# Performance work log

Measured on AMD Instinct MI355X. Metric: run time of the kernel, lower is better.

Reference implementation:

```python
import jax, jax.numpy as jnp
import numpy as np

# Config matching init_kwargs (single TP rank: local heads == total heads)
HID = 1024
NH = 16      # query heads
NKV = 4      # kv heads (GQA)
HD = 64      # head_dim
B = 2
S = 2048
SCALE = 1.0 / HD ** 0.5


def setup_inputs() -> dict:
    key = jax.random.key(0)
    k1, k2, k3 = jax.random.split(key, 3)
    qkv_out = (NH + 2 * NKV) * HD  # 1536
    return {
        "hidden_states": jax.random.normal(k1, (B, S, HID), dtype=jnp.float32),
        "W_qkv": jax.random.normal(k2, (HID, qkv_out), dtype=jnp.float32) * 0.02,
        "W_o": jax.random.normal(k3, (HID, HID), dtype=jnp.float32) * 0.02,
    }


def reference(hidden_states, W_qkv, W_o):
    b, s, _ = hidden_states.shape
    rep = NH // NKV  # GQA repeat factor (repeat_interleave: q head h uses kv group h // rep)

    qkv = hidden_states @ W_qkv  # [B, S, (NH+2*NKV)*HD]
    q, k, v = jnp.split(qkv, [NH * HD, (NH + NKV) * HD], axis=-1)

    # [B, heads, S, HD]
    q = q.reshape(b, s, NH, HD).transpose(0, 2, 1, 3)
    k = k.reshape(b, s, NKV, HD).transpose(0, 2, 1, 3)
    v = v.reshape(b, s, NKV, HD).transpose(0, 2, 1, 3)

    # Group query heads by shared kv head instead of repeat_interleaving K/V in memory.
    qg = q.reshape(b, NKV, rep, s, HD)  # head h = g*rep + r  <=>  kv group g = h // rep
    scores = jnp.einsum("bgrqd,bgkd->bgrqk", qg, k) * SCALE  # [B, NKV, rep, S, S]

    # Causal mask (prefill path: kv_cache is None, seq_len > 1)
    causal = jnp.triu(jnp.ones((s, s), dtype=bool), k=1)
    scores = jnp.where(causal, jnp.finfo(scores.dtype).min, scores)

    attn = jax.nn.softmax(scores, axis=-1)
    out = jnp.einsum("bgrqk,bgkd->bgrqd", attn, v)  # [B, NKV, rep, S, HD]
    out = out.reshape(b, NH, s, HD).transpose(0, 2, 1, 3).reshape(b, s, NH * HD)
    return out @ W_o  # [B, S, HID]
```

## Files before the change

### kernel.cpp

```cpp
#include <hip/hip_runtime.h>
#include <stdint.h>

using u16 = unsigned short;
using u32 = unsigned int;

typedef __attribute__((ext_vector_type(8))) short short8;
typedef __attribute__((ext_vector_type(4))) float f32x4;
typedef __attribute__((ext_vector_type(16))) float f32x16;

__device__ __forceinline__ u16 f2bf(float f) {
  u32 u = __builtin_bit_cast(u32, f);
  u = (u + 0x7fffu + ((u >> 16) & 1u)) >> 16;
  return (u16)u;
}

__device__ __forceinline__ u32 cvtpk(float lo, float hi) {
  u32 r;
  asm("v_cvt_pk_bf16_f32 %0, %1, %2" : "=v"(r) : "v"(lo), "v"(hi));
  return r;
}

__device__ __forceinline__ short8 ld16(const u16* p) {
  uint4 v = *(const uint4*)p;
  union { uint4 u; short8 s; } c; c.u = v; return c.s;
}

__device__ __forceinline__ void gload_lds16(const void* g, void* l) {
  __builtin_amdgcn_global_load_lds(
      (const __attribute__((address_space(1))) void*)g,
      (__attribute__((address_space(3))) void*)l, 16, 0, 0);
}

__device__ __forceinline__ f32x16 mfma32(short8 a, short8 b, f32x16 c) {
  return __builtin_amdgcn_mfma_f32_32x32x16_bf16(a, b, c, 0, 0, 0);
}

__global__ __launch_bounds__(256) void k_prep(const float* __restrict__ hs,
                                              const float* __restrict__ wqkv,
                                              const float* __restrict__ wo,
                                              u16* __restrict__ hsb,
                                              u16* __restrict__ wqkvT,
                                              u16* __restrict__ woT) {
  __shared__ float tile[32][33];
  const int bid = blockIdx.x;
  if (bid < 4096) {
    int i = bid * 256 + threadIdx.x;
    float4 v = ((const float4*)hs)[i];
    ushort4 o;
    o.x = f2bf(v.x); o.y = f2bf(v.y); o.z = f2bf(v.z); o.w = f2bf(v.w);
    ((ushort4*)hsb)[i] = o;
    return;
  }
  const float* in; u16* out; int R, C, bx, by;
  if (bid < 5632) {
    int idx = bid - 4096;
    in = wqkv; out = wqkvT; R = 1024; C = 1536;
    bx = idx % 48; by = idx / 48;
  } else {
    int idx = bid - 5632;
    in = wo; out = woT; R = 1024; C = 1024;
    bx = idx & 31; by = idx >> 5;
  }
  int c0 = bx * 32, r0 = by * 32;
  int tx = threadIdx.x & 31, ty = threadIdx.x >> 5;
#pragma unroll
  for (int i = 0; i < 4; ++i) {
    int r = ty + 8 * i;
    tile[r][tx] = in[(size_t)(r0 + r) * C + c0 + tx];
  }
  __syncthreads();
#pragma unroll
  for (int i = 0; i < 4; ++i) {
    int r = ty + 8 * i;
    out[(size_t)(c0 + r) * R + r0 + tx] = f2bf(tile[tx][r]);
  }
}

__global__ __launch_bounds__(256, 3) void k_gemm_qkv(
    const u16* __restrict__ A, const u16* __restrict__ BT,
    u16* __restrict__ qb, u16* __restrict__ kb, u16* __restrict__ vbT) {
  const int K = 1024;
  __shared__ __align__(16) u16 As[2][64 * 64];
  __shared__ __align__(16) u16 Bs[2][128 * 64];
  const int t = threadIdx.x;
  const int l = t & 63;
  const int wid = t >> 6;
  const int wr = wid >> 1, wc = wid & 1;
  const int lr = l & 15, lg = l >> 4;
  const int cpx = (int)gridDim.x >> 3;
  const int nb = (blockIdx.x & 7) * cpx + ((int)blockIdx.x >> 3);
  const int mt = nb / 12, nt = nb % 12;
  const int m0 = mt << 6, n0 = nt << 7;

  f32x4 zero = {0.f, 0.f, 0.f, 0.f};
  f32x4 acc[2][4];
#pragma unroll
  for (int i = 0; i < 2; ++i)
#pragma unroll
    for (int j = 0; j < 4; ++j) acc[i][j] = zero;

  const u16* Ab = A + (size_t)m0 * K;
  const u16* Bb = BT + (size_t)n0 * K;

  auto STAGE = [&](int kt, int bsel) {
    const u16* Ak = Ab + kt * 64;
    const u16* Bk = Bb + kt * 64;
#pragma unroll
    for (int i = 0; i < 2; ++i) {
      int o16 = i * 256 + t;
      int row = o16 >> 3, c = o16 & 7;
      int sc = c ^ (row & 7);
      gload_lds16(Ak + (size_t)row * K + sc * 8, &As[bsel][o16 * 8]);
    }
#pragma unroll
    for (int i = 0; i < 4; ++i) {
      int o16 = i * 256 + t;
      int row = o16 >> 3, c = o16 & 7;
      int sc = c ^ (row & 7);
      gload_lds16(Bk + (size_t)row * K + sc * 8, &Bs[bsel][o16 * 8]);
    }
  };

  STAGE(0, 0);
  asm volatile("s_waitcnt vmcnt(0)" ::: "memory");
  __builtin_amdgcn_s_barrier();

  for (int kt = 0; kt < 16; ++kt) {
    const int cur = kt & 1;
    if (kt + 1 < 16) STAGE(kt + 1, cur ^ 1);
#pragma unroll
    for (int ks = 0; ks < 2; ++ks) {
      short8 a[2], b[4];
#pragma unroll
      for (int mi = 0; mi < 2; ++mi) {
        int row = wr * 32 + mi * 16 + lr;
        int c = (ks * 4 + lg) ^ (row & 7);
        a[mi] = ld16(&As[cur][(row * 8 + c) * 8]);
      }
#pragma unroll
      for (int ni = 0; ni < 4; ++ni) {
        int row = wc * 64 + ni * 16 + lr;
        int c = (ks * 4 + lg) ^ (row & 7);
        b[ni] = ld16(&Bs[cur][(row * 8 + c) * 8]);
      }
#pragma unroll
      for (int mi = 0; mi < 2; ++mi)
#pragma unroll
        for (int ni = 0; ni < 4; ++ni)
          acc[mi][ni] = __builtin_amdgcn_mfma_f32_16x16x32_bf16(a[mi], b[ni], acc[mi][ni], 0, 0, 0);
    }
    asm volatile("s_waitcnt vmcnt(0)" ::: "memory");
    __builtin_amdgcn_s_barrier();
    asm volatile("" ::: "memory");
  }

#pragma unroll
  for (int mi = 0; mi < 2; ++mi) {
#pragma unroll
    for (int ni = 0; ni < 4; ++ni) {
#pragma unroll
      for (int r = 0; r < 4; ++r) {
        float v = acc[mi][ni][r];
        int m = m0 + wr * 32 + mi * 16 + 4 * lg + r;
        int n = n0 + wc * 64 + ni * 16 + lr;
        int bb = m >> 11, s = m & 2047;
        int tau = s >> 5, i32e = s & 31;
        if (n < 1024) {
          int h = n >> 6, d = n & 63;
          int kc = d >> 4, hi2 = (d >> 3) & 1, e = d & 7;
          qb[((size_t)(bb * 16 + h)) * 131072 +
             (size_t)((tau * 4 + kc) * 64 + (hi2 << 5 | i32e)) * 8 + e] = f2bf(v * 0.18033688f);
        } else if (n < 1280) {
          int g = (n - 1024) >> 6, d = n & 63;
          int kc = d >> 4, hi2 = (d >> 3) & 1, e = d & 7;
          kb[((size_t)(bb * 4 + g)) * 131072 +
             (size_t)((tau * 4 + kc) * 64 + (hi2 << 5 | i32e)) * 8 + e] = f2bf(v);
        } else {
          int g = (n - 1280) >> 6, dT = n & 63;
          int c = (s >> 4) & 1, hi2 = (s >> 3) & 1, e = s & 7;
          int dd = dT >> 5, i32v = dT & 31;
          vbT[((size_t)(bb * 4 + g)) * 131072 +
              (size_t)(((tau * 2 + dd) * 2 + c) * 64 + (hi2 << 5 | i32v)) * 8 + e] = f2bf(v);
        }
      }
    }
  }
}

__global__ __launch_bounds__(256, 2) void k_gemm_out(
    const u16* __restrict__ A, const u16* __restrict__ BT, float* __restrict__ out) {
  const int K = 1024, N = 1024;
  __shared__ __align__(16) u16 As[2][64 * 64];
  __shared__ __align__(16) u16 Bs[2][128 * 64];
  const int t = threadIdx.x;
  const int l = t & 63;
  const int wid = t >> 6;
  const int wr = wid >> 1, wc = wid & 1;
  const int lr = l & 15, lg = l >> 4;
  const int cpx = (int)gridDim.x >> 3;
  const int nb = (blockIdx.x & 7) * cpx + ((int)blockIdx.x >> 3);
  const int mt = nb >> 3, nt = nb & 7;
  const int m0 = mt << 6, n0 = nt << 7;

  f32x4 zero = {0.f, 0.f, 0.f, 0.f};
  f32x4 acc[2][4];
#pragma unroll
  for (int i = 0; i < 2; ++i)
#pragma unroll
    for (int j = 0; j < 4; ++j) acc[i][j] = zero;

  const u16* Ab = A + (size_t)m0 * K;
  const u16* Bb = BT + (size_t)n0 * K;

  auto STAGE = [&](int kt, int bsel) {
    const u16* Ak = Ab + kt * 64;
    const u16* Bk = Bb + kt * 64;
#pragma unroll
    for (int i = 0; i < 2; ++i) {
      int o16 = i * 256 + t;
      int row = o16 >> 3, c = o16 & 7;
      int sc = c ^ (row & 7);
      gload_lds16(Ak + (size_t)row * K + sc * 8, &As[bsel][o16 * 8]);
    }
#pragma unroll
    for (int i = 0; i < 4; ++i) {
      int o16 = i * 256 + t;
      int row = o16 >> 3, c = o16 & 7;
      int sc = c ^ (row & 7);
      gload_lds16(Bk + (size_t)row * K + sc * 8, &Bs[bsel][o16 * 8]);
    }
  };

  STAGE(0, 0);
  asm volatile("s_waitcnt vmcnt(0)" ::: "memory");
  __builtin_amdgcn_s_barrier();

  for (int kt = 0; kt < 16; ++kt) {
    const int cur = kt & 1;
    if (kt + 1 < 16) STAGE(kt + 1, cur ^ 1);
#pragma unroll
    for (int ks = 0; ks < 2; ++ks) {
      short8 a[2], b[4];
#pragma unroll
      for (int mi = 0; mi < 2; ++mi) {
        int row = wr * 32 + mi * 16 + lr;
        int c = (ks * 4 + lg) ^ (row & 7);
        a[mi] = ld16(&As[cur][(row * 8 + c) * 8]);
      }
#pragma unroll
      for (int ni = 0; ni < 4; ++ni) {
        int row = wc * 64 + ni * 16 + lr;
        int c = (ks * 4 + lg) ^ (row & 7);
        b[ni] = ld16(&Bs[cur][(row * 8 + c) * 8]);
      }
#pragma unroll
      for (int mi = 0; mi < 2; ++mi)
#pragma unroll
        for (int ni = 0; ni < 4; ++ni)
          acc[mi][ni] = __builtin_amdgcn_mfma_f32_16x16x32_bf16(a[mi], b[ni], acc[mi][ni], 0, 0, 0);
    }
    asm volatile("s_waitcnt vmcnt(0)" ::: "memory");
    __builtin_amdgcn_s_barrier();
    asm volatile("" ::: "memory");
  }

#pragma unroll
  for (int mi = 0; mi < 2; ++mi)
#pragma unroll
    for (int ni = 0; ni < 4; ++ni)
#pragma unroll
      for (int r = 0; r < 4; ++r) {
        int m = m0 + wr * 32 + mi * 16 + 4 * lg + r;
        int n = n0 + wc * 64 + ni * 16 + lr;
        out[(size_t)m * N + n] = acc[mi][ni][r];
      }
}

__global__ __launch_bounds__(256, 2) void k_attn(const u16* __restrict__ qbuf,
                                                 const u16* __restrict__ kbuf,
                                                 const u16* __restrict__ vbuf,
                                                 u16* __restrict__ attn) {
  const int t = threadIdx.x;
  const int l = t & 63, wid = t >> 6;
  const int i32 = l & 31, hi = l >> 5;
  const int bh = blockIdx.x >> 4;
  const int t16 = blockIdx.x & 15;
  const int b = bh >> 4, h = bh & 15, g = h >> 2;
  const int qt = (wid == 0) ? t16 : (wid == 1) ? 31 - t16 : (wid == 2) ? 32 + t16 : 63 - t16;
  const int q0 = qt * 32;
  const int nblk = (q0 >> 6) + 1;

  const u16* qp = qbuf + ((size_t)(b * 16 + h)) * 131072;
  const u16* kp = kbuf + ((size_t)(b * 4 + g)) * 131072;
  const u16* vp = vbuf + ((size_t)(b * 4 + g)) * 131072;

  short8 qf[4];
#pragma unroll
  for (int kc = 0; kc < 4; ++kc)
    qf[kc] = ld16(qp + ((size_t)((q0 >> 5) * 4 + kc) * 64 + l) * 8);

  f32x16 z16 = {0.f, 0.f, 0.f, 0.f, 0.f, 0.f, 0.f, 0.f,
                0.f, 0.f, 0.f, 0.f, 0.f, 0.f, 0.f, 0.f};
  f32x16 o[2];
  o[0] = z16; o[1] = z16;
  float lsum = 0.f;

  short8 kA[2][4], kB[2][4];

  auto LOADK = [&](short8(&kf)[2][4], int kv0) {
#pragma unroll
    for (int mf = 0; mf < 2; ++mf)
#pragma unroll
      for (int kc = 0; kc < 4; ++kc)
        kf[mf][kc] = ld16(kp + ((size_t)((((kv0 >> 5) + mf) * 4 + kc)) * 64 + l) * 8);
  };

  auto PROCESS = [&](short8(&kf)[2][4], short8(&kn)[2][4], bool pref, int kv0, bool last) {
    short8 vf[2][2][2];
#pragma unroll
    for (int mf = 0; mf < 2; ++mf)
#pragma unroll
      for (int dd = 0; dd < 2; ++dd)
#pragma unroll
        for (int c = 0; c < 2; ++c)
          vf[dd][mf][c] = ld16(vp + ((size_t)((((kv0 >> 5) + mf) * 2 + dd) * 2 + c) * 64 + l) * 8);

    f32x16 sc[2];
    __builtin_amdgcn_s_setprio(1);
    sc[0] = mfma32(kf[0][0], qf[0], z16);
    sc[1] = mfma32(kf[1][0], qf[0], z16);
#pragma unroll
    for (int kc = 1; kc < 4; ++kc) {
      sc[0] = mfma32(kf[0][kc], qf[kc], sc[0]);
      sc[1] = mfma32(kf[1][kc], qf[kc], sc[1]);
    }
    __builtin_amdgcn_s_setprio(0);

    if (pref) LOADK(kn, kv0 + 64);

    if (last) {
      const int iloc = (q0 - kv0) + i32;
#pragma unroll
      for (int mf = 0; mf < 2; ++mf)
#pragma unroll
        for (int R = 0; R < 16; ++R) {
          int j = 32 * mf + (R & 3) + 8 * (R >> 2) + 4 * hi;
          if (j > iloc) sc[mf][R] = -1e30f;
        }
    }

    float s0 = 0.f, s1 = 0.f, s2 = 0.f, s3 = 0.f;
#pragma unroll
    for (int mf = 0; mf < 2; ++mf)
#pragma unroll
      for (int R = 0; R < 16; R += 4) {
        float p0 = __builtin_amdgcn_exp2f(sc[mf][R]);
        float p1 = __builtin_amdgcn_exp2f(sc[mf][R + 1]);
        float p2 = __builtin_amdgcn_exp2f(sc[mf][R + 2]);
        float p3 = __builtin_amdgcn_exp2f(sc[mf][R + 3]);
        sc[mf][R] = p0; sc[mf][R + 1] = p1; sc[mf][R + 2] = p2; sc[mf][R + 3] = p3;
        s0 += p0; s1 += p1; s2 += p2; s3 += p3;
      }
    lsum += (s0 + s1) + (s2 + s3);

    short8 pb[2][2];
#pragma unroll
    for (int mf = 0; mf < 2; ++mf)
#pragma unroll
      for (int c = 0; c < 2; ++c) {
        union { u32 w[4]; short8 s8; } U;
#pragma unroll
        for (int q = 0; q < 2; ++q) {
          u32 wa = cvtpk(sc[mf][8 * c + 2 * q], sc[mf][8 * c + 2 * q + 1]);
          u32 wb = cvtpk(sc[mf][8 * c + 4 + 2 * q], sc[mf][8 * c + 4 + 2 * q + 1]);
          auto rr = __builtin_amdgcn_permlane32_swap(wa, wb, false, false);
          U.w[q] = (u32)rr[0];
          U.w[2 + q] = (u32)rr[1];
        }
        pb[mf][c] = U.s8;
      }

    __builtin_amdgcn_s_setprio(1);
#pragma unroll
    for (int mf = 0; mf < 2; ++mf)
#pragma unroll
      for (int c = 0; c < 2; ++c) {
        o[0] = mfma32(vf[0][mf][c], pb[mf][c], o[0]);
        o[1] = mfma32(vf[1][mf][c], pb[mf][c], o[1]);
      }
    __builtin_amdgcn_s_setprio(0);
  };

  LOADK(kA, 0);
  int kv0 = 0, blk = 0;
  while (true) {
    PROCESS(kA, kB, blk + 1 < nblk, kv0, blk == nblk - 1);
    ++blk; kv0 += 64;
    if (blk >= nblk) break;
    PROCESS(kB, kA, blk + 1 < nblk, kv0, blk == nblk - 1);
    ++blk; kv0 += 64;
    if (blk >= nblk) break;
  }

  float tot;
  {
    u32 su = __builtin_bit_cast(u32, lsum);
    auto rr = __builtin_amdgcn_permlane32_swap(su, su, false, false);
    tot = __builtin_bit_cast(float, (u32)rr[0]) + __builtin_bit_cast(float, (u32)rr[1]);
  }
  float inv = 1.f / tot;
  u16* ao = attn + ((size_t)(b * 2048 + q0)) * 1024 + h * 64;
#pragma unroll
  for (int dd = 0; dd < 2; ++dd) {
#pragma unroll
    for (int R = 0; R < 16; R += 2) {
      int d = dd * 32 + (R & 3) + 8 * (R >> 2) + 4 * hi;
      u32 w = cvtpk(o[dd][R] * inv, o[dd][R + 1] * inv);
      *(u32*)(ao + (size_t)i32 * 1024 + d) = w;
    }
  }
}

extern "C" void kernel_launch(void* const* d_in, const int* in_sizes, int n_in,
                              void* d_out, int out_size, void* d_ws, size_t ws_size,
                              hipStream_t stream) {
  const float* hs = (const float*)d_in[0];
  const float* wqkv = (const float*)d_in[1];
  const float* wo = (const float*)d_in[2];
  float* out = (float*)d_out;
  u16* ws = (u16*)d_ws;

  u16* hsb = ws;
  u16* wqkvT = hsb + 4194304;
  u16* woT = wqkvT + 1572864;
  u16* qb = woT + 1048576;
  u16* kb = qb + 4194304;
  u16* vb = kb + 1048576;
  u16* attn = vb + 1048576;
  (void)in_sizes; (void)n_in; (void)out_size; (void)ws_size;

  k_prep<<<6656, 256, 0, stream>>>(hs, wqkv, wo, hsb, wqkvT, woT);
  k_gemm_qkv<<<768, 256, 0, stream>>>(hsb, wqkvT, qb, kb, vb);
  k_attn<<<512, 256, 0, stream>>>(qb, kb, vb, attn);
  k_gemm_out<<<512, 256, 0, stream>>>(attn, woT, out);
}
```

Before: 84.56 us.

## Balance causal attention work by splitting paired query tiles across wave pairs

Reassigns query tiles so each pair of waves handles a short tile and its long mirror tile, splitting the long tile's KV range between the two waves. Partial unnormalized outputs and row sums are combined through shared memory before normalization and store. This aims to remove the load imbalance where one wave in a block processed far more KV blocks than the others. It adds LDS usage and a block-wide barrier.

```diff
diff --git a/kernel.cpp b/kernel.cpp
--- a/kernel.cpp
+++ b/kernel.cpp
@@ -280,32 +280,37 @@
                                                  const u16* __restrict__ kbuf,
                                                  const u16* __restrict__ vbuf,
                                                  u16* __restrict__ attn) {
+  __shared__ float osh[2][2048];
+  __shared__ float lsh[2][64];
   const int t = threadIdx.x;
   const int l = t & 63, wid = t >> 6;
   const int i32 = l & 31, hi = l >> 5;
   const int bh = blockIdx.x >> 4;
-  const int t16 = blockIdx.x & 15;
+  const int j = blockIdx.x & 15;
   const int b = bh >> 4, h = bh & 15, g = h >> 2;
-  const int qt = (wid == 0) ? t16 : (wid == 1) ? 31 - t16 : (wid == 2) ? 32 + t16 : 63 - t16;
-  const int q0 = qt * 32;
-  const int nblk = (q0 >> 6) + 1;
+  const int slot = wid >> 1, w01 = wid & 1;
+  const int a = j + slot * 16;
+  const int qta = a, qtb = 63 - a;
+  const int A = (a >> 1) + 1;
+  const int Bn = 33 - A;
+  const int split = 17 - A;
 
   const u16* qp = qbuf + ((size_t)(b * 16 + h)) * 131072;
   const u16* kp = kbuf + ((size_t)(b * 4 + g)) * 131072;
   const u16* vp = vbuf + ((size_t)(b * 4 + g)) * 131072;
 
-  short8 qf[4];
-#pragma unroll
-  for (int kc = 0; kc < 4; ++kc)
-    qf[kc] = ld16(qp + ((size_t)((q0 >> 5) * 4 + kc) * 64 + l) * 8);
-
   f32x16 z16 = {0.f, 0.f, 0.f, 0.f, 0.f, 0.f, 0.f, 0.f,
                 0.f, 0.f, 0.f, 0.f, 0.f, 0.f, 0.f, 0.f};
+  short8 qf[4];
   f32x16 o[2];
-  o[0] = z16; o[1] = z16;
-  float lsum = 0.f;
-
+  float lsum;
   short8 kA[2][4], kB[2][4];
+
+  auto LOADQ = [&](int qt) {
+#pragma unroll
+    for (int kc = 0; kc < 4; ++kc)
+      qf[kc] = ld16(qp + ((size_t)(qt * 4 + kc) * 64 + l) * 8);
+  };
 
   auto LOADK = [&](short8(&kf)[2][4], int kv0) {
 #pragma unroll
@@ -315,7 +320,8 @@
         kf[mf][kc] = ld16(kp + ((size_t)((((kv0 >> 5) + mf) * 4 + kc)) * 64 + l) * 8);
   };
 
-  auto PROCESS = [&](short8(&kf)[2][4], short8(&kn)[2][4], bool pref, int kv0, bool last) {
+  auto PROCESS = [&](short8(&kf)[2][4], short8(&kn)[2][4], bool pref, int kv0, bool last,
+                     int q0loc) {
     short8 vf[2][2][2];
 #pragma unroll
     for (int mf = 0; mf < 2; ++mf)
@@ -339,13 +345,13 @@
     if (pref) LOADK(kn, kv0 + 64);
 
     if (last) {
-      const int iloc = (q0 - kv0) + i32;
+      const int iloc = (q0loc - kv0) + i32;
 #pragma unroll
       for (int mf = 0; mf < 2; ++mf)
 #pragma unroll
         for (int R = 0; R < 16; ++R) {
-          int j = 32 * mf + (R & 3) + 8 * (R >> 2) + 4 * hi;
-          if (j > iloc) sc[mf][R] = -1e30f;
+          int j2 = 32 * mf + (R & 3) + 8 * (R >> 2) + 4 * hi;
+          if (j2 > iloc) sc[mf][R] = -1e30f;
         }
     }
 
@@ -391,33 +397,77 @@
     __builtin_amdgcn_s_setprio(0);
   };
 
-  LOADK(kA, 0);
-  int kv0 = 0, blk = 0;
-  while (true) {
-    PROCESS(kA, kB, blk + 1 < nblk, kv0, blk == nblk - 1);
-    ++blk; kv0 += 64;
-    if (blk >= nblk) break;
-    PROCESS(kB, kA, blk + 1 < nblk, kv0, blk == nblk - 1);
-    ++blk; kv0 += 64;
-    if (blk >= nblk) break;
-  }
-
-  float tot;
-  {
-    u32 su = __builtin_bit_cast(u32, lsum);
-    auto rr = __builtin_amdgcn_permlane32_swap(su, su, false, false);
-    tot = __builtin_bit_cast(float, (u32)rr[0]) + __builtin_bit_cast(float, (u32)rr[1]);
-  }
-  float inv = 1.f / tot;
-  u16* ao = attn + ((size_t)(b * 2048 + q0)) * 1024 + h * 64;
-#pragma unroll
-  for (int dd = 0; dd < 2; ++dd) {
-#pragma unroll
-    for (int R = 0; R < 16; R += 2) {
-      int d = dd * 32 + (R & 3) + 8 * (R >> 2) + 4 * hi;
-      u32 w = cvtpk(o[dd][R] * inv, o[dd][R + 1] * inv);
-      *(u32*)(ao + (size_t)i32 * 1024 + d) = w;
-    }
+  auto RUN = [&](int qt, int n0, int n1) {
+    LOADQ(qt);
+    const int q0loc = qt * 32;
+    const int nbq = (qt >> 1) + 1;
+    LOADK(kA, n0 * 64);
+    int n = n0;
+    while (true) {
+      PROCESS(kA, kB, n + 1 < n1, n * 64, n == nbq - 1, q0loc);
+      if (++n >= n1) break;
+      PROCESS(kB, kA, n + 1 < n1, n * 64, n == nbq - 1, q0loc);
+      if (++n >= n1) break;
+    }
+  };
+
+  auto STORE = [&](int qt) {
+    float tot;
+    {
+      u32 su = __builtin_bit_cast(u32, lsum);
+      auto rr = __builtin_amdgcn_permlane32_swap(su, su, false, false);
+      tot = __builtin_bit_cast(float, (u32)rr[0]) + __builtin_bit_cast(float, (u32)rr[1]);
+    }
+    float inv = 1.f / tot;
+    u16* ao = attn + ((size_t)(b * 2048 + qt * 32)) * 1024 + h * 64;
+#pragma unroll
+    for (int dd = 0; dd < 2; ++dd) {
+#pragma unroll
+      for (int R = 0; R < 16; R += 2) {
+        int d = dd * 32 + (R & 3) + 8 * (R >> 2) + 4 * hi;
+        u32 w = cvtpk(o[dd][R] * inv, o[dd][R + 1] * inv);
+        *(u32*)(ao + (size_t)i32 * 1024 + d) = w;
+      }
+    }
+  };
+
+  o[0] = z16; o[1] = z16; lsum = 0.f;
+  if (w01 == 0) {
+    RUN(qta, 0, A);
+    STORE(qta);
+    o[0] = z16; o[1] = z16; lsum = 0.f;
+    RUN(qtb, 0, split);
+    float* dst = &osh[slot][0];
+#pragma unroll
+    for (int dd = 0; dd < 2; ++dd) {
+      float4* d4 = (float4*)&dst[(dd * 64 + l) * 16];
+#pragma unroll
+      for (int q = 0; q < 4; ++q) {
+        float4 v4;
+        v4.x = o[dd][4 * q]; v4.y = o[dd][4 * q + 1];
+        v4.z = o[dd][4 * q + 2]; v4.w = o[dd][4 * q + 3];
+        d4[q] = v4;
+      }
+    }
+    lsh[slot][l] = lsum;
+  } else {
+    RUN(qtb, split, Bn);
+  }
+  __syncthreads();
+  if (w01 == 1) {
+    const float* src = &osh[slot][0];
+#pragma unroll
+    for (int dd = 0; dd < 2; ++dd) {
+      const float4* s4 = (const float4*)&src[(dd * 64 + l) * 16];
+#pragma unroll
+      for (int q = 0; q < 4; ++q) {
+        float4 v4 = s4[q];
+        o[dd][4 * q] += v4.x; o[dd][4 * q + 1] += v4.y;
+        o[dd][4 * q + 2] += v4.z; o[dd][4 * q + 3] += v4.w;
+      }
+    }
+    lsum += lsh[slot][l];
+    STORE(qtb);
   }
 }
 
```

Result: no change. 84.91 us (+0.4%).

## Fuse hidden-state bf16 conversion into QKV GEMM and restructure attention loop

Applied to the files above, without the earlier changes.

The separate fp32-to-bf16 conversion pass over hidden_states is dropped. The QKV GEMM now loads fp32 A tiles into registers, converts them with v_cvt_pk_bf16_f32, and writes them to swizzled LDS after the MFMA work. This removes one kernel pass's global write and re-read, at the cost of more register pressure and the extra fp32 read traffic now landing inside the GEMM. Separately, the attention inner loop processes two KV blocks per iteration with explicit K/V loads, replacing cross-iteration K prefetch and changing how latency is hidden.

```diff
diff --git a/kernel.cpp b/kernel.cpp
--- a/kernel.cpp
+++ b/kernel.cpp
@@ -35,29 +35,18 @@
   return __builtin_amdgcn_mfma_f32_32x32x16_bf16(a, b, c, 0, 0, 0);
 }
 
-__global__ __launch_bounds__(256) void k_prep(const float* __restrict__ hs,
-                                              const float* __restrict__ wqkv,
+__global__ __launch_bounds__(256) void k_prep(const float* __restrict__ wqkv,
                                               const float* __restrict__ wo,
-                                              u16* __restrict__ hsb,
                                               u16* __restrict__ wqkvT,
                                               u16* __restrict__ woT) {
   __shared__ float tile[32][33];
   const int bid = blockIdx.x;
-  if (bid < 4096) {
-    int i = bid * 256 + threadIdx.x;
-    float4 v = ((const float4*)hs)[i];
-    ushort4 o;
-    o.x = f2bf(v.x); o.y = f2bf(v.y); o.z = f2bf(v.z); o.w = f2bf(v.w);
-    ((ushort4*)hsb)[i] = o;
-    return;
-  }
   const float* in; u16* out; int R, C, bx, by;
-  if (bid < 5632) {
-    int idx = bid - 4096;
+  if (bid < 1536) {
     in = wqkv; out = wqkvT; R = 1024; C = 1536;
-    bx = idx % 48; by = idx / 48;
+    bx = bid % 48; by = bid / 48;
   } else {
-    int idx = bid - 5632;
+    int idx = bid - 1536;
     in = wo; out = woT; R = 1024; C = 1024;
     bx = idx & 31; by = idx >> 5;
   }
@@ -77,7 +66,7 @@
 }
 
 __global__ __launch_bounds__(256, 3) void k_gemm_qkv(
-    const u16* __restrict__ A, const u16* __restrict__ BT,
+    const float* __restrict__ hsF, const u16* __restrict__ BT,
     u16* __restrict__ qb, u16* __restrict__ kb, u16* __restrict__ vbT) {
   const int K = 1024;
   __shared__ __align__(16) u16 As[2][64 * 64];
@@ -99,19 +88,31 @@
 #pragma unroll
     for (int j = 0; j < 4; ++j) acc[i][j] = zero;
 
-  const u16* Ab = A + (size_t)m0 * K;
+  const float* Ab = hsF + (size_t)m0 * K;
   const u16* Bb = BT + (size_t)n0 * K;
 
-  auto STAGE = [&](int kt, int bsel) {
-    const u16* Ak = Ab + kt * 64;
+  auto LOADA = [&](int kt, float4(&ar)[4]) {
+#pragma unroll
+    for (int i = 0; i < 4; ++i) {
+      int idx = i * 256 + t;
+      int row = idx >> 4, h2 = idx & 15;
+      ar[i] = *(const float4*)(Ab + (size_t)row * K + kt * 64 + h2 * 4);
+    }
+  };
+  auto WRITEA = [&](int bsel, float4(&ar)[4]) {
+#pragma unroll
+    for (int i = 0; i < 4; ++i) {
+      int idx = i * 256 + t;
+      int row = idx >> 4, h2 = idx & 15;
+      int c = h2 >> 1, half = h2 & 1;
+      u32 w0 = cvtpk(ar[i].x, ar[i].y);
+      u32 w1 = cvtpk(ar[i].z, ar[i].w);
+      u32* dst = (u32*)&As[bsel][(row * 8 + (c ^ (row & 7))) * 8 + half * 4];
+      dst[0] = w0; dst[1] = w1;
+    }
+  };
+  auto STAGEB = [&](int kt, int bsel) {
     const u16* Bk = Bb + kt * 64;
-#pragma unroll
-    for (int i = 0; i < 2; ++i) {
-      int o16 = i * 256 + t;
-      int row = o16 >> 3, c = o16 & 7;
-      int sc = c ^ (row & 7);
-      gload_lds16(Ak + (size_t)row * K + sc * 8, &As[bsel][o16 * 8]);
-    }
 #pragma unroll
     for (int i = 0; i < 4; ++i) {
       int o16 = i * 256 + t;
@@ -121,13 +122,22 @@
     }
   };
 
-  STAGE(0, 0);
-  asm volatile("s_waitcnt vmcnt(0)" ::: "memory");
+  {
+    float4 ar[4];
+    LOADA(0, ar);
+    STAGEB(0, 0);
+    WRITEA(0, ar);
+  }
+  asm volatile("s_waitcnt vmcnt(0) lgkmcnt(0)" ::: "memory");
   __builtin_amdgcn_s_barrier();
 
   for (int kt = 0; kt < 16; ++kt) {
     const int cur = kt & 1;
-    if (kt + 1 < 16) STAGE(kt + 1, cur ^ 1);
+    float4 ar[4];
+    if (kt + 1 < 16) {
+      LOADA(kt + 1, ar);
+      STAGEB(kt + 1, cur ^ 1);
+    }
 #pragma unroll
     for (int ks = 0; ks < 2; ++ks) {
       short8 a[2], b[4];
@@ -149,7 +159,8 @@
         for (int ni = 0; ni < 4; ++ni)
           acc[mi][ni] = __builtin_amdgcn_mfma_f32_16x16x32_bf16(a[mi], b[ni], acc[mi][ni], 0, 0, 0);
     }
-    asm volatile("s_waitcnt vmcnt(0)" ::: "memory");
+    if (kt + 1 < 16) WRITEA(cur ^ 1, ar);
+    asm volatile("s_waitcnt vmcnt(0) lgkmcnt(0)" ::: "memory");
     __builtin_amdgcn_s_barrier();
     asm volatile("" ::: "memory");
   }
@@ -305,8 +316,6 @@
   o[0] = z16; o[1] = z16;
   float lsum = 0.f;
 
-  short8 kA[2][4], kB[2][4];
-
   auto LOADK = [&](short8(&kf)[2][4], int kv0) {
 #pragma unroll
     for (int mf = 0; mf < 2; ++mf)
@@ -314,9 +323,7 @@
       for (int kc = 0; kc < 4; ++kc)
         kf[mf][kc] = ld16(kp + ((size_t)((((kv0 >> 5) + mf) * 4 + kc)) * 64 + l) * 8);
   };
-
-  auto PROCESS = [&](short8(&kf)[2][4], short8(&kn)[2][4], bool pref, int kv0, bool last) {
-    short8 vf[2][2][2];
+  auto LOADV = [&](short8(&vf)[2][2][2], int kv0) {
 #pragma unroll
     for (int mf = 0; mf < 2; ++mf)
 #pragma unroll
@@ -324,8 +331,8 @@
 #pragma unroll
         for (int c = 0; c < 2; ++c)
           vf[dd][mf][c] = ld16(vp + ((size_t)((((kv0 >> 5) + mf) * 2 + dd) * 2 + c) * 64 + l) * 8);
-
-    f32x16 sc[2];
+  };
+  auto QK = [&](f32x16(&sc)[2], short8(&kf)[2][4]) {
     __builtin_amdgcn_s_setprio(1);
     sc[0] = mfma32(kf[0][0], qf[0], z16);
     sc[1] = mfma32(kf[1][0], qf[0], z16);
@@ -335,20 +342,18 @@
       sc[1] = mfma32(kf[1][kc], qf[kc], sc[1]);
     }
     __builtin_amdgcn_s_setprio(0);
-
-    if (pref) LOADK(kn, kv0 + 64);
-
-    if (last) {
-      const int iloc = (q0 - kv0) + i32;
-#pragma unroll
-      for (int mf = 0; mf < 2; ++mf)
-#pragma unroll
-        for (int R = 0; R < 16; ++R) {
-          int j = 32 * mf + (R & 3) + 8 * (R >> 2) + 4 * hi;
-          if (j > iloc) sc[mf][R] = -1e30f;
-        }
-    }
-
+  };
+  auto MASK = [&](f32x16(&sc)[2], int kv0) {
+    const int iloc = (q0 - kv0) + i32;
+#pragma unroll
+    for (int mf = 0; mf < 2; ++mf)
+#pragma unroll
+      for (int R = 0; R < 16; ++R) {
+        int j2 = 32 * mf + (R & 3) + 8 * (R >> 2) + 4 * hi;
+        if (j2 > iloc) sc[mf][R] = -1e30f;
+      }
+  };
+  auto EXPSUM = [&](f32x16(&sc)[2]) {
     float s0 = 0.f, s1 = 0.f, s2 = 0.f, s3 = 0.f;
 #pragma unroll
     for (int mf = 0; mf < 2; ++mf)
@@ -362,7 +367,8 @@
         s0 += p0; s1 += p1; s2 += p2; s3 += p3;
       }
     lsum += (s0 + s1) + (s2 + s3);
-
+  };
+  auto PACKPV = [&](f32x16(&sc)[2], short8(&vf)[2][2][2]) {
     short8 pb[2][2];
 #pragma unroll
     for (int mf = 0; mf < 2; ++mf)
@@ -379,7 +385,6 @@
         }
         pb[mf][c] = U.s8;
       }
-
     __builtin_amdgcn_s_setprio(1);
 #pragma unroll
     for (int mf = 0; mf < 2; ++mf)
@@ -391,15 +396,37 @@
     __builtin_amdgcn_s_setprio(0);
   };
 
-  LOADK(kA, 0);
-  int kv0 = 0, blk = 0;
-  while (true) {
-    PROCESS(kA, kB, blk + 1 < nblk, kv0, blk == nblk - 1);
-    ++blk; kv0 += 64;
-    if (blk >= nblk) break;
-    PROCESS(kB, kA, blk + 1 < nblk, kv0, blk == nblk - 1);
-    ++blk; kv0 += 64;
-    if (blk >= nblk) break;
+  int n = 0;
+  while (n + 2 <= nblk) {
+    const int kv0 = n * 64;
+    short8 kf0[2][4], kf1[2][4];
+    LOADK(kf0, kv0);
+    LOADK(kf1, kv0 + 64);
+    short8 vf0[2][2][2];
+    LOADV(vf0, kv0);
+    f32x16 sc0[2], sc1[2];
+    QK(sc0, kf0);
+    QK(sc1, kf1);
+    short8 vf1[2][2][2];
+    LOADV(vf1, kv0 + 64);
+    if (n + 1 == nblk - 1) MASK(sc1, kv0 + 64);
+    EXPSUM(sc0);
+    EXPSUM(sc1);
+    PACKPV(sc0, vf0);
+    PACKPV(sc1, vf1);
+    n += 2;
+  }
+  if (n < nblk) {
+    const int kv0 = n * 64;
+    short8 kf0[2][4];
+    LOADK(kf0, kv0);
+    short8 vf0[2][2][2];
+    LOADV(vf0, kv0);
+    f32x16 sc0[2];
+    QK(sc0, kf0);
+    MASK(sc0, kv0);
+    EXPSUM(sc0);
+    PACKPV(sc0, vf0);
   }
 
   float tot;
@@ -430,8 +457,7 @@
   float* out = (float*)d_out;
   u16* ws = (u16*)d_ws;
 
-  u16* hsb = ws;
-  u16* wqkvT = hsb + 4194304;
+  u16* wqkvT = ws;
   u16* woT = wqkvT + 1572864;
   u16* qb = woT + 1048576;
   u16* kb = qb + 4194304;
@@ -439,8 +465,8 @@
   u16* attn = vb + 1048576;
   (void)in_sizes; (void)n_in; (void)out_size; (void)ws_size;
 
-  k_prep<<<6656, 256, 0, stream>>>(hs, wqkv, wo, hsb, wqkvT, woT);
-  k_gemm_qkv<<<768, 256, 0, stream>>>(hsb, wqkvT, qb, kb, vb);
+  k_prep<<<2560, 256, 0, stream>>>(wqkv, wo, wqkvT, woT);
+  k_gemm_qkv<<<768, 256, 0, stream>>>(hs, wqkvT, qb, kb, vb);
   k_attn<<<512, 256, 0, stream>>>(qb, kb, vb, attn);
   k_gemm_out<<<512, 256, 0, stream>>>(attn, woT, out);
 }
```

Result: slower. 89.25 us (+5.5%).
